# Kernel optimization log

Hardware: AMD Instinct MI355X
Metric: run time of the kernel (lower is better)

Reference implementation:

```python
import jax, jax.numpy as jnp
import numpy as np

B, L, T = 128, 400, 30
E, He, Hd, A, V = 300, 512, 512, 512, 20000
PAD_ID, UNK_ID, SOS_ID = 0, 1, 2


def setup_inputs() -> dict:
    key = jax.random.key(0)
    ks = jax.random.split(key, 20)
    f = lambda k, shape, s=0.05: jax.random.normal(k, shape, jnp.float32) * s
    return {
        "enc_outputs": jax.random.normal(ks[0], (B, L, He), jnp.float32),
        "s": jax.random.normal(ks[1], (B, Hd), jnp.float32),
        "source_WORD_encoding": jax.random.randint(ks[2], (B, L), 0, V),
        "target_WORD_encoding": jax.random.randint(ks[3], (B, T), 0, V),
        "embed": f(ks[4], (V, E)),
        "W_ih": f(ks[5], (3 * Hd, E + He)),
        "b_ih": jnp.zeros((3 * Hd,), jnp.float32),
        "W_hh": f(ks[6], (3 * Hd, Hd)),
        "b_hh": jnp.zeros((3 * Hd,), jnp.float32),
        "att_Wh": f(ks[7], (A, He)),
        "att_Ws": f(ks[8], (A, Hd)),
        "att_b": jnp.zeros((A,), jnp.float32),
        "att_v": f(ks[9], (A,)),
        "copy_W": f(ks[10], (1, He + Hd)),
        "copy_b": jnp.zeros((1,), jnp.float32),
        "read_W": f(ks[11], (Hd, E + He + Hd)),
        "read_b": jnp.zeros((Hd,), jnp.float32),
        "read_Wo": f(ks[12], (V, Hd // 2)),
    }


def reference(enc_outputs, s, source_WORD_encoding, target_WORD_encoding,
              embed, W_ih, b_ih, W_hh, b_hh, att_Wh, att_Ws, att_b, att_v,
              copy_W, copy_b, read_W, read_b, read_Wo):
    pad_mask = source_WORD_encoding == PAD_ID          # [B, L]
    # Precompute encoder projection for Bahdanau attention (same math each step)
    enc_proj = jnp.einsum('ble,ae->bla', enc_outputs, att_Wh)  # [B, L, A]
    word0 = jnp.full((enc_outputs.shape[0],), SOS_ID, jnp.int32)
    ctx0 = jnp.zeros((enc_outputs.shape[0], He), enc_outputs.dtype)

    def step(carry, tgt_t):
        s, ctx, word = carry
        emb = embed[word]                               # [B, E]
        x = jnp.concatenate([emb, ctx], axis=1)         # [B, E+He]
        gi = x @ W_ih.T + b_ih
        gh = s @ W_hh.T + b_hh
        ir, iz, in_ = jnp.split(gi, 3, axis=1)
        hr, hz, hn = jnp.split(gh, 3, axis=1)
        r = jax.nn.sigmoid(ir + hr)
        z = jax.nn.sigmoid(iz + hz)
        n = jnp.tanh(in_ + r * hn)
        s_new = (1.0 - z) * n + z * s                   # GRUCell
        # Bahdanau attention
        q = s_new @ att_Ws.T + att_b                    # [B, A]
        e = jnp.einsum('bla,a->bl', jnp.tanh(enc_proj + q[:, None, :]), att_v)
        e = jnp.where(pad_mask, -jnp.inf, e)
        attn = jax.nn.softmax(e, axis=1)                # [B, L]
        ctx_new = jnp.einsum('bl,ble->be', attn, enc_outputs)
        # Copy switch
        p_copy = jax.nn.sigmoid(jnp.concatenate([s_new, ctx_new], 1) @ copy_W.T + copy_b)
        # Readout (tie=False): Linear -> Maxout(2) -> Wo
        rvec = jnp.concatenate([emb, ctx_new, s_new], 1) @ read_W.T + read_b
        m = rvec.reshape(rvec.shape[0], Hd // 2, 2).max(-1)
        energy = m @ read_Wo.T                          # [B, V]
        p_vocab = jax.nn.softmax(energy, axis=1)
        p_out = jnp.concatenate([(1.0 - p_copy) * p_vocab, p_copy * attn], 1) + 1e-12
        log_p = jnp.log(p_out)                          # [B, V+L]
        next_word = jnp.where(tgt_t >= V, UNK_ID, tgt_t).astype(jnp.int32)
        return (s_new, ctx_new, next_word), log_p

    _, log_ps = jax.lax.scan(step, (s, ctx0, word0), target_WORD_encoding.T.astype(jnp.int32))
    return jnp.transpose(log_ps, (1, 0, 2))             # [B, T, V+L]
```

## Files before the change

kernel.cpp:

```cpp
#include <hip/hip_runtime.h>

typedef unsigned short u16;
typedef unsigned int u32;
typedef short bf16x8 __attribute__((ext_vector_type(8)));
typedef float f32x4 __attribute__((ext_vector_type(4)));

#define NB 128
#define NL 400
#define NT 30
#define NE 300
#define KE 320
#define NHE 512
#define NHD 512
#define NA 512
#define NV 20000
#define NVP 20096
#define K1 1024
#define N1 2048
#define NW 2048
#define OUTW (NV+NL)
#define NBLK 512

static __device__ __forceinline__ u16 f2b(float x){ u32 u=__float_as_uint(x); u += 0x7FFFu + ((u>>16)&1u); return (u16)(u>>16); }
static __device__ __forceinline__ float b2f(u16 h){ return __uint_as_float(((u32)h)<<16); }
static __device__ __forceinline__ float fsig(float x){ return 1.f/(1.f+__expf(-x)); }
static __device__ __forceinline__ float ftanh(float x){ return 1.f - 2.f/(__expf(2.f*x)+1.f); }

static __device__ __forceinline__ float atL(const float* p){ return __hip_atomic_load(p, __ATOMIC_RELAXED, __HIP_MEMORY_SCOPE_AGENT); }
static __device__ __forceinline__ u32   atLu(const u32* p){ return __hip_atomic_load(p, __ATOMIC_RELAXED, __HIP_MEMORY_SCOPE_AGENT); }
static __device__ __forceinline__ void  atS(float* p, float v){ __hip_atomic_store(p, v, __ATOMIC_RELAXED, __HIP_MEMORY_SCOPE_AGENT); }
static __device__ __forceinline__ void  atSu(u32* p, u32 v){ __hip_atomic_store(p, v, __ATOMIC_RELAXED, __HIP_MEMORY_SCOPE_AGENT); }

static __device__ __forceinline__ void gll16(const u16* g, u16* l){
  __builtin_amdgcn_global_load_lds((const __attribute__((address_space(1))) void*)g,
                                   (__attribute__((address_space(3))) void*)l, 16, 0, 0);
}

static __device__ __forceinline__ void gemm_pipe(const u16* A, int lda, const u16* Bm, int ldb,
                                                 int K, u16* ls, f32x4 (&acc)[4][4]){
  const int tid = threadIdx.x;
  const int wave = tid>>6, lane = tid&63;
  const int srow = lane>>2;
  const int sko = (((lane&3) ^ ((lane>>3)&3)))*8;
  const int wm = wave>>1, wn = wave&1;
#pragma unroll
  for (int i=0;i<4;i++)
#pragma unroll
    for (int j=0;j<4;j++)
#pragma unroll
      for (int q=0;q<4;q++) acc[i][j][q] = 0.f;
  const int nk = K>>5;
  auto issue = [&](int kt, int bsel){
    u16* dA = ls + bsel*8192;
    u16* dB = dA + 4096;
#pragma unroll
    for (int i=0;i<2;i++){
      const int c = wave*2+i;
      const int row = c*16 + srow;
      gll16(A + (size_t)row*lda + kt + sko, dA + c*512);
      gll16(Bm + (size_t)row*ldb + kt + sko, dB + c*512);
    }
  };
  issue(0, 0);
  issue(nk>1 ? 32 : 0, 1);
  for (int it=0; it<nk; ++it){
    asm volatile("s_waitcnt vmcnt(4)" ::: "memory");
    __builtin_amdgcn_s_barrier();
    const u16* lsA = ls + (it&1)*8192;
    const u16* lsB = lsA + 4096;
    const int rsel = (lane&15)*32 + (((lane>>4) ^ ((lane>>1)&3))*8);
    bf16x8 aF[4], bF[4];
#pragma unroll
    for (int mi=0;mi<4;mi++) aF[mi] = *(const bf16x8*)(lsA + (wm*64+mi*16)*32 + rsel);
#pragma unroll
    for (int nj=0;nj<4;nj++) bF[nj] = *(const bf16x8*)(lsB + (wn*64+nj*16)*32 + rsel);
#pragma unroll
    for (int mi=0;mi<4;mi++)
#pragma unroll
      for (int nj=0;nj<4;nj++)
        acc[mi][nj] = __builtin_amdgcn_mfma_f32_16x16x32_bf16(aF[mi], bF[nj], acc[mi][nj], 0,0,0);
    __builtin_amdgcn_s_barrier();
    issue(it+2 < nk ? (it+2)*32 : 0, it&1);
  }
  asm volatile("s_waitcnt vmcnt(0)" ::: "memory");
  __builtin_amdgcn_s_barrier();
}


__global__ __launch_bounds__(256) void k_conv_flat(const float* __restrict__ s, u16* __restrict__ d, long n){
  long i = (long)blockIdx.x*256 + threadIdx.x;
  const long st = (long)gridDim.x*256;
  for (; i<n; i+=st) d[i] = f2b(s[i]);
}

__global__ __launch_bounds__(256) void k_convpad(const float* __restrict__ s, u16* __restrict__ d,
                                                 int srows, int sk, int dk, long total){
  long i = (long)blockIdx.x*256 + threadIdx.x;
  const long st = (long)gridDim.x*256;
  for (; i<total; i+=st){
    int r = (int)(i / dk), k = (int)(i - (long)r*dk);
    d[i] = (r < srows && k < sk) ? f2b(s[(size_t)r*sk + k]) : (u16)0;
  }
}

__global__ __launch_bounds__(512) void k_transpose(const float* __restrict__ enc, u16* __restrict__ encT){
  const int b = blockIdx.y, jt = blockIdx.x;
  __shared__ float tile[16][33];
  const int tid = threadIdx.x;
  for (int lt=0; lt<25; lt++){
    {
      int l = lt*16 + (tid>>5), j = jt*32 + (tid&31);
      tile[tid>>5][tid&31] = enc[((size_t)b*NL + l)*512 + j];
    }
    __syncthreads();
    {
      int jw = tid>>4, lw = tid&15;
      encT[((size_t)b*512 + jt*32 + jw)*NL + lt*16 + lw] = f2b(tile[lw][jw]);
    }
    __syncthreads();
  }
}

__global__ __launch_bounds__(256) void k_build_w1(const float* __restrict__ Whh, const float* __restrict__ Wih, u16* __restrict__ d){
  int idx = blockIdx.x*256 + threadIdx.x;
  if (idx >= N1*K1) return;
  int n = idx >> 10, k = idx & 1023;
  float v = 0.f;
  if (n < 1024)       v = (k<512) ? Whh[(size_t)n*512 + k] : Wih[(size_t)n*812 + 300 + (k-512)];
  else if (n < 1536)  v = (k<512) ? Whh[(size_t)n*512 + k] : 0.f;
  else                v = (k<512) ? 0.f : Wih[(size_t)(n-512)*812 + 300 + (k-512)];
  d[idx] = f2b(v);
}

__global__ __launch_bounds__(256) void k_build_w2(const float* __restrict__ Wr, u16* __restrict__ d){
  int idx = blockIdx.x*256 + threadIdx.x;
  if (idx >= 512*K1) return;
  int r = idx >> 10, k = idx & 1023;
  float v = (k<512) ? Wr[(size_t)r*1324 + 812 + k] : Wr[(size_t)r*1324 + 300 + (k-512)];
  d[idx] = f2b(v);
}

__global__ __launch_bounds__(256) void k_build_wemb(const float* __restrict__ Wih, const float* __restrict__ Wr, u16* __restrict__ d){
  int idx = blockIdx.x*256 + threadIdx.x;
  if (idx >= NW*KE) return;
  int n = idx / KE, k = idx - n*KE;
  float v = 0.f;
  if (k < NE) v = (n < 1536) ? Wih[(size_t)n*812 + k] : Wr[(size_t)(n-1536)*1324 + k];
  d[idx] = f2b(v);
}

__global__ __launch_bounds__(256) void k_build_xemb(const int* __restrict__ tgt, const float* __restrict__ embed, u16* __restrict__ d){
  int idx = blockIdx.x*256 + threadIdx.x;
  if (idx >= NT*NB*KE) return;
  int row = idx / KE, k = idx - row*KE;
  int t = row >> 7, b = row & 127;
  u16 hv = 0;
  if (k < NE){
    int w = 2;
    if (t > 0){ w = tgt[b*NT + t-1]; if ((u32)w >= (u32)NV) w = 1; }
    hv = f2b(embed[(size_t)w*NE + k]);
  }
  d[idx] = hv;
}

__global__ __launch_bounds__(256) void k_init(const float* __restrict__ s_in, float* __restrict__ sbuf0, u16* __restrict__ x1A){
  int idx = blockIdx.x*256 + threadIdx.x;
  if (idx < 65536){
    int b = idx>>9, j = idx&511;
    float v = s_in[idx];
    sbuf0[idx] = v;
    x1A[(size_t)b*K1 + j] = f2b(v);
  } else if (idx < 131072){
    int k = idx - 65536;
    int b = k>>9, j = k&511;
    x1A[(size_t)b*K1 + 512 + j] = 0;
  }
}

__global__ __launch_bounds__(256) void k_encproj(const u16* __restrict__ A, const u16* __restrict__ Bw, u16* __restrict__ C){
  __shared__ __align__(16) u16 ls[16384];
  const int n0 = blockIdx.x*128, m0 = blockIdx.y*128;
  f32x4 acc[4][4];
  gemm_pipe(A + (size_t)m0*512, 512, Bw + (size_t)n0*512, 512, 512, ls, acc);
  const int tid=threadIdx.x, wave=tid>>6, lane=tid&63, wm=wave>>1, wn=wave&1;
#pragma unroll
  for (int mi=0;mi<4;mi++)
#pragma unroll
    for (int nj=0;nj<4;nj++)
#pragma unroll
      for (int q=0;q<4;q++){
        int r = m0 + wm*64 + mi*16 + (lane>>4)*4 + q;
        int c = n0 + wn*64 + nj*16 + (lane&15);
        C[(size_t)r*512 + c] = f2b(acc[mi][nj][q]);
      }
}

__global__ __launch_bounds__(256) void k_gemm_emb(const u16* __restrict__ Xe, const u16* __restrict__ We, float* __restrict__ gre){
  __shared__ __align__(16) u16 ls[16384];
  const int n0 = blockIdx.x*128, m0 = blockIdx.y*128;
  f32x4 acc[4][4];
  gemm_pipe(Xe + (size_t)m0*KE, KE, We + (size_t)n0*KE, KE, KE, ls, acc);
  const int tid=threadIdx.x, wave=tid>>6, lane=tid&63, wm=wave>>1, wn=wave&1;
#pragma unroll
  for (int mi=0;mi<4;mi++)
#pragma unroll
    for (int nj=0;nj<4;nj++)
#pragma unroll
      for (int q=0;q<4;q++){
        int r = m0 + wm*64 + mi*16 + (lane>>4)*4 + q;
        int c = n0 + wn*64 + nj*16 + (lane&15);
        gre[(size_t)r*NW + c] = acc[mi][nj][q];
      }
}


struct KP {
  const float *bih, *bhh, *attb, *attv, *copyW, *copyb;
  const int   *src;
  const u16   *Wsb, *eproj, *encT, *W1;
  const float *gre;
  float *gA, *gB, *sbufA, *sbufB, *e, *ctx_ws, *attn_all, *pcb_all;
  u16   *x1A;
  u32   *slots, *gen;
};

static __device__ __forceinline__ void gbar(const KP& p, u32& ep){
  ++ep;
  asm volatile("s_waitcnt vmcnt(0)" ::: "memory");
  __syncthreads();
  if (threadIdx.x==0)
    atSu(p.slots + blockIdx.x, ep);
  if (blockIdx.x==0){
    if (threadIdx.x < 64){
      const u32* sl = p.slots + threadIdx.x*8;
      for (;;){
        u32 mn = 0xFFFFFFFFu;
#pragma unroll
        for (int j=0;j<8;j++){
          u32 v = atLu(sl+j);
          mn = v<mn ? v : mn;
        }
        if (__all(mn >= ep)) break;
        __builtin_amdgcn_s_sleep(4);
      }
      atSu(p.gen + threadIdx.x*16, ep);
    }
  } else if (threadIdx.x==0){
    const u32* gp = p.gen + (blockIdx.x>>3)*16;
    while (atLu(gp) < ep) __builtin_amdgcn_s_sleep(4);
  }
  asm volatile("" ::: "memory");
  __syncthreads();
}

static __device__ void ph_g1(const KP& p, char* sm, int u, int t){
  u16* ls = (u16*)sm;
  const int ks = u&1, n0 = (u>>1)*128;
  const u16* A  = p.x1A + (size_t)t*NB*K1 + ks*512;
  const u16* Bm = p.W1 + (size_t)n0*K1 + ks*512;
  f32x4 acc[4][4];
  gemm_pipe(A, K1, Bm, K1, 512, ls, acc);
  float* gd = ks ? p.gB : p.gA;
  const int tid=threadIdx.x, wave=tid>>6, lane=tid&63, wm=wave>>1, wn=wave&1;
#pragma unroll
  for (int mi=0;mi<4;mi++)
#pragma unroll
    for (int nj=0;nj<4;nj++)
#pragma unroll
      for (int q=0;q<4;q++){
        int r = wm*64 + mi*16 + (lane>>4)*4 + q;
        int c = n0 + wn*64 + nj*16 + (lane&15);
        atS(gd + (size_t)r*N1 + c, acc[mi][nj][q]);
      }
}

static __device__ void ph_gqe(const KP& p, char* sm, int blk, int t){
  const int tid = threadIdx.x;
  const int b = blk>>2, yq = blk&3;
  float* s_lds = (float*)sm;
  float* q_lds = s_lds + 512;
  const float* gAb = p.gA + (size_t)b*N1;
  const float* gBb = p.gB + (size_t)b*N1;
  const float* ge = p.gre + (size_t)(t*NB + b)*NW;
  const float* s_old = (t&1) ? p.sbufB : p.sbufA;
  float* s_new       = (t&1) ? p.sbufA : p.sbufB;
  u16* x1n = p.x1A + (size_t)(t+1)*NB*K1 + (size_t)b*K1;
#pragma unroll
  for (int h=0; h<2; h++){
    const int j = tid + h*256;
    float g0 = atL(gAb + j)      + atL(gBb + j);
    float g1 = atL(gAb + 512+j)  + atL(gBb + 512+j);
    float g2 = atL(gAb + 1024+j) + atL(gBb + 1024+j);
    float g3 = atL(gAb + 1536+j) + atL(gBb + 1536+j);
    float r = fsig(g0 + ge[j] + p.bih[j] + p.bhh[j]);
    float z = fsig(g1 + ge[512+j] + p.bih[512+j] + p.bhh[512+j]);
    float n = ftanh(ge[1024+j] + g3 + p.bih[1024+j] + r*(g2 + p.bhh[1024+j]));
    float sn = (1.f-z)*n + z*atL(s_old + (size_t)b*512 + j);
    s_lds[j] = sn;
    if (yq==0){
      atS(s_new + (size_t)b*512 + j, sn);
      u32 me = f2b(sn);
      u32 oth = (u32)__shfl_xor((int)me, 1);
      if (!(tid&1)) atSu((u32*)(x1n + j), me | (oth<<16));
    }
  }
  __syncthreads();
  {
    const int al = tid>>1, kh = tid&1;
    const int a = yq*128 + al;
    const u16* wr = p.Wsb + (size_t)a*512 + kh*256;
    const float* sp = s_lds + kh*256;
    float acc = 0.f;
#pragma unroll 8
    for (int k=0;k<256;k+=8){
      bf16x8 w = *(const bf16x8*)(wr + k);
#pragma unroll
      for (int j=0;j<8;j++) acc += sp[k+j]*b2f((u16)w[j]);
    }
    acc += __shfl_xor(acc, 1);
    if (kh==0) q_lds[al] = acc + p.attb[a];
  }
  __syncthreads();
  const int lane = tid&63, wv = tid>>6;
  const int g16 = lane>>4, sub = lane&15;
  const int gid = wv*4 + g16;
  float v8[8], q8[8];
#pragma unroll
  for (int j=0;j<8;j++){
    v8[j] = p.attv[yq*128 + sub*8 + j];
    q8[j] = q_lds[sub*8 + j];
  }
  float* epo = p.e + ((size_t)yq*NB + b)*NL;
#pragma unroll 5
  for (int i=0;i<25;i++){
    const int l = i*16 + gid;
    const u16* ep = p.eproj + ((size_t)b*NL + l)*512 + yq*128 + sub*8;
    bf16x8 w8 = *(const bf16x8*)ep;
    float acc = 0.f;
#pragma unroll
    for (int j8=0;j8<8;j8++) acc += v8[j8]*ftanh(b2f((u16)w8[j8]) + q8[j8]);
    acc += __shfl_xor(acc,1); acc += __shfl_xor(acc,2);
    acc += __shfl_xor(acc,4); acc += __shfl_xor(acc,8);
    if (sub==0) atS(epo + l, acc);
  }
}

static __device__ void ph_smctx(const KP& p, char* sm, int blk, int t){
  const int tid = threadIdx.x;
  const int b = blk>>2, jq = blk&3;
  const int lane = tid&63, wv = tid>>6;
  float* a_lds = (float*)sm;
  float* red   = (float*)(sm+1600);
  float* bc    = (float*)(sm+1664);
  float s0 = atL(p.e + (size_t)b*NL + tid)
           + atL(p.e + ((size_t)NB + b)*NL + tid)
           + atL(p.e + ((size_t)2*NB + b)*NL + tid)
           + atL(p.e + ((size_t)3*NB + b)*NL + tid);
  float ev0 = (p.src[b*NL + tid]!=0) ? s0 : -INFINITY;
  float ev1 = -INFINITY;
  if (tid < NL-256){
    float s1 = atL(p.e + (size_t)b*NL + tid+256)
             + atL(p.e + ((size_t)NB + b)*NL + tid+256)
             + atL(p.e + ((size_t)2*NB + b)*NL + tid+256)
             + atL(p.e + ((size_t)3*NB + b)*NL + tid+256);
    ev1 = (p.src[b*NL + tid+256]!=0) ? s1 : -INFINITY;
  }
  float mx = fmaxf(ev0, ev1);
  for (int off=32; off; off>>=1) mx = fmaxf(mx, __shfl_xor(mx, off));
  if (lane==0) red[wv]=mx;
  __syncthreads();
  if (tid==0) bc[0] = fmaxf(fmaxf(red[0],red[1]), fmaxf(red[2],red[3]));
  __syncthreads();
  const float M = bc[0];
  float p0 = (ev0==-INFINITY)? 0.f : __expf(ev0 - M);
  float p1 = (ev1==-INFINITY)? 0.f : __expf(ev1 - M);
  float sm2 = p0 + p1;
  for (int off=32; off; off>>=1) sm2 += __shfl_xor(sm2, off);
  if (lane==0) red[wv]=sm2;
  __syncthreads();
  if (tid==0) bc[1] = red[0]+red[1]+red[2]+red[3];
  __syncthreads();
  const float inv = 1.f / bc[1];
  a_lds[tid] = p0*inv;
  if (tid < NL-256) a_lds[tid+256] = p1*inv;
  __syncthreads();
  if (jq==0){
    float* ab = p.attn_all + ((size_t)t*NB + b)*NL;
    ab[tid] = a_lds[tid];
    if (tid < NL-256) ab[tid+256] = a_lds[tid+256];
  }
  const int j = jq*128 + (tid>>1), lh = tid&1;
  const u16* er = p.encT + ((size_t)b*512 + j)*NL + lh*200;
  const float* ap = a_lds + lh*200;
  float acc = 0.f;
#pragma unroll 5
  for (int m=0;m<200;m+=8){
    bf16x8 e8 = *(const bf16x8*)(er + m);
#pragma unroll
    for (int jj=0;jj<8;jj++) acc += ap[m+jj]*b2f((u16)e8[jj]);
  }
  acc += __shfl_xor(acc, 1);
  u32 me = f2b(acc);
  u32 oth = (u32)__shfl_xor((int)me, 2);
  if ((tid&3)==0)
    atSu((u32*)(p.x1A + (size_t)(t+1)*NB*K1 + (size_t)b*K1 + 512 + j), me | (oth<<16));
  if (!(tid&1)) atS(p.ctx_ws + (size_t)b*512 + j, acc);
}

static __device__ void ph_pcopy(const KP& p, int u, int t){
  const int tid = threadIdx.x;
  const float* sN = (t&1) ? p.sbufA : p.sbufB;
  const int b = u*32 + (tid>>3), kq = tid&7;
  const float* v = (kq<4) ? (sN + (size_t)b*512 + kq*128) : (p.ctx_ws + (size_t)b*512 + (kq-4)*128);
  const float* w = p.copyW + kq*128;
  float acc = 0.f;
#pragma unroll 8
  for (int k=0;k<128;k++) acc += atL(v+k)*w[k];
  acc += __shfl_xor(acc,1); acc += __shfl_xor(acc,2); acc += __shfl_xor(acc,4);
  if (kq==0) p.pcb_all[(size_t)t*NB + b] = fsig(acc + p.copyb[0]);
}

__global__ __launch_bounds__(256,2) void k_persist(KP p){
  __shared__ __align__(16) char sm[33024];
  const int blk = blockIdx.x;
  u32 ep = 0;
  for (int t=0; t<NT; ++t){
    if (blk < 32) ph_g1(p, sm, blk, t);
    else if (blk < 36){ if (t > 0) ph_pcopy(p, blk-32, t-1); }
    gbar(p, ep);
    ph_gqe(p, sm, blk, t);
    gbar(p, ep);
    ph_smctx(p, sm, blk, t);
    gbar(p, ep);
  }
  if (blk < 4) ph_pcopy(p, blk, NT-1);
}


__global__ __launch_bounds__(256) void kB_read(const u16* __restrict__ x1A, const u16* __restrict__ W2,
    const float* __restrict__ gre, const float* __restrict__ readb, u16* __restrict__ mbf_all){
  __shared__ __align__(16) u16 ls[16384];
  const int t = blockIdx.y, n0 = blockIdx.x*128;
  const u16* A = x1A + (size_t)(t+1)*NB*K1;
  f32x4 acc[4][4];
  gemm_pipe(A, K1, W2 + (size_t)n0*K1, K1, K1, ls, acc);
  const int tid=threadIdx.x, wave=tid>>6, lane=tid&63, wm=wave>>1, wn=wave&1;
#pragma unroll
  for (int mi=0;mi<4;mi++)
#pragma unroll
    for (int nj=0;nj<4;nj++)
#pragma unroll
      for (int q=0;q<4;q++){
        int r = wm*64 + mi*16 + (lane>>4)*4 + q;
        int c = n0 + wn*64 + nj*16 + (lane&15);
        float v = acc[mi][nj][q] + readb[c] + gre[((size_t)(t*NB + r))*NW + 1536 + c];
        float o = __shfl_xor(v, 1);
        float mx2 = fmaxf(v, o);
        if (!(lane&1)) mbf_all[(size_t)(t*NB + r)*256 + (c>>1)] = f2b(mx2);
      }
}

__global__ __launch_bounds__(256) void kB_lse(const u16* __restrict__ mbf_all, const u16* __restrict__ WoP,
    float* __restrict__ parts){
  __shared__ __align__(16) u16 ls[16384];
  __shared__ float psum[128][2];
  const int t = blockIdx.y, n0 = blockIdx.x*128;
  f32x4 acc[4][4];
  gemm_pipe(mbf_all + (size_t)t*NB*256, 256, WoP + (size_t)n0*256, 256, 256, ls, acc);
  const int tid=threadIdx.x, wave=tid>>6, lane=tid&63, wm=wave>>1, wn=wave&1;
  float rs[4][4];
#pragma unroll
  for (int mi=0;mi<4;mi++)
#pragma unroll
    for (int q=0;q<4;q++) rs[mi][q]=0.f;
#pragma unroll
  for (int mi=0;mi<4;mi++)
#pragma unroll
    for (int nj=0;nj<4;nj++){
      const int c = n0 + wn*64 + nj*16 + (lane&15);
#pragma unroll
      for (int q=0;q<4;q++)
        if (c < NV) rs[mi][q] += __expf(acc[mi][nj][q]);
    }
#pragma unroll
  for (int mi=0;mi<4;mi++)
#pragma unroll
    for (int q=0;q<4;q++){
      float v = rs[mi][q];
      v += __shfl_xor(v,1); v += __shfl_xor(v,2); v += __shfl_xor(v,4); v += __shfl_xor(v,8);
      if ((lane&15)==0) psum[wm*64 + mi*16 + (lane>>4)*4 + q][wn] = v;
    }
  __syncthreads();
  if (tid < 128) parts[(size_t)(t*NB + tid)*160 + blockIdx.x] = psum[tid][0] + psum[tid][1];
}

__global__ __launch_bounds__(256) void kB_lsered(const float* __restrict__ parts, float* __restrict__ LSE_all){
  const int row = blockIdx.x, tid = threadIdx.x;
  const int lane = tid&63, wv = tid>>6;
  __shared__ float red[4];
  float v = (tid<157)? parts[(size_t)row*160 + tid] : 0.f;
  for (int off=32; off; off>>=1) v += __shfl_xor(v, off);
  if (lane==0) red[wv]=v;
  __syncthreads();
  if (tid==0) LSE_all[row] = __logf(red[0]+red[1]+red[2]+red[3]);
}

__global__ __launch_bounds__(256) void kB_out2(const u16* __restrict__ mbf_all, const u16* __restrict__ WoP,
    const float* __restrict__ LSE_all, const float* __restrict__ pcb_all, float* __restrict__ out){
  __shared__ __align__(16) u16 ls[16384];
  const int t = blockIdx.y, n0 = blockIdx.x*128;
  f32x4 acc[4][4];
  gemm_pipe(mbf_all + (size_t)t*NB*256, 256, WoP + (size_t)n0*256, 256, 256, ls, acc);
  const int tid=threadIdx.x, wave=tid>>6, lane=tid&63, wm=wave>>1, wn=wave&1;
  float lse_r[4][4], lo_r[4][4];
#pragma unroll
  for (int mi=0;mi<4;mi++)
#pragma unroll
    for (int q=0;q<4;q++){
      const int r = wm*64 + mi*16 + (lane>>4)*4 + q;
      lse_r[mi][q] = LSE_all[(size_t)t*NB + r];
      lo_r[mi][q]  = 1.f - pcb_all[(size_t)t*NB + r];
    }
#pragma unroll
  for (int mi=0;mi<4;mi++)
#pragma unroll
    for (int nj=0;nj<4;nj++){
      const int c = n0 + wn*64 + nj*16 + (lane&15);
      if (c >= NV) continue;
#pragma unroll
      for (int q=0;q<4;q++){
        const int r = wm*64 + mi*16 + (lane>>4)*4 + q;
        out[((size_t)r*NT + t)*OUTW + c] = __logf(lo_r[mi][q]*__expf(acc[mi][nj][q]-lse_r[mi][q]) + 1e-12f);
      }
    }
}

__global__ __launch_bounds__(256) void kB_copy(const float* __restrict__ pcb_all, const float* __restrict__ attn_all,
    float* __restrict__ out){
  const int total = NT*NB*NL;
  for (int idx = blockIdx.x*256 + threadIdx.x; idx < total; idx += gridDim.x*256){
    int t = idx / (NB*NL);
    int rem = idx - t*(NB*NL);
    int b = rem / NL, l = rem - b*NL;
    float pc = pcb_all[(size_t)t*NB + b];
    float av = attn_all[((size_t)t*NB + b)*NL + l];
    out[((size_t)b*NT + t)*OUTW + NV + l] = __logf(pc*av + 1e-12f);
  }
}


extern "C" void kernel_launch(void* const* d_in, const int* in_sizes, int n_in,
                              void* d_out, int out_size, void* d_ws, size_t ws_size,
                              hipStream_t stream){
  const float* enc   = (const float*)d_in[0];
  const float* s_in  = (const float*)d_in[1];
  const int*   src   = (const int*)d_in[2];
  const int*   tgt   = (const int*)d_in[3];
  const float* embed = (const float*)d_in[4];
  const float* W_ih  = (const float*)d_in[5];
  const float* b_ih  = (const float*)d_in[6];
  const float* W_hh  = (const float*)d_in[7];
  const float* b_hh  = (const float*)d_in[8];
  const float* attWh = (const float*)d_in[9];
  const float* attWs = (const float*)d_in[10];
  const float* attb  = (const float*)d_in[11];
  const float* attv  = (const float*)d_in[12];
  const float* copyW = (const float*)d_in[13];
  const float* copyb = (const float*)d_in[14];
  const float* readW = (const float*)d_in[15];
  const float* readb = (const float*)d_in[16];
  const float* readWo= (const float*)d_in[17];
  float* out = (float*)d_out;
  (void)in_sizes; (void)n_in; (void)out_size; (void)ws_size;

  char* wsp = (char*)d_ws;
  size_t off = 0;
  auto alloc = [&](size_t bytes)->char*{ char* p = wsp + off; off = (off + bytes + 255) & ~(size_t)255; return p; };
  u16* enc_bf    = (u16*)alloc((size_t)NB*NL*NHE*2);
  u16* encT      = (u16*)alloc((size_t)NB*NHE*NL*2);
  u16* eproj     = (u16*)alloc((size_t)NB*NL*NA*2);
  u16* attWh_bf  = (u16*)alloc((size_t)NA*NHE*2);
  u16* Wsb       = (u16*)alloc((size_t)NA*NHD*2);
  u16* W1        = (u16*)alloc((size_t)N1*K1*2);
  u16* W2        = (u16*)alloc((size_t)512*K1*2);
  u16* Wemb      = (u16*)alloc((size_t)NW*KE*2);
  u16* Xemb      = (u16*)alloc((size_t)NT*NB*KE*2);
  u16* WoP       = (u16*)alloc((size_t)NVP*256*2);
  float* gre     = (float*)alloc((size_t)NT*NB*NW*4);
  float* gA      = (float*)alloc((size_t)NB*N1*4);
  float* gB      = (float*)alloc((size_t)NB*N1*4);
  u16* x1A       = (u16*)alloc((size_t)(NT+1)*NB*K1*2);
  float* sbufA   = (float*)alloc((size_t)NB*NHD*4);
  float* sbufB   = (float*)alloc((size_t)NB*NHD*4);
  float* e_buf   = (float*)alloc((size_t)4*NB*NL*4);
  float* attn_all= (float*)alloc((size_t)NT*NB*NL*4);
  float* ctx_ws  = (float*)alloc((size_t)NB*NHE*4);
  u16* mbf_all   = (u16*)alloc((size_t)NT*NB*256*2);
  float* parts   = (float*)alloc((size_t)NT*NB*160*4);
  float* LSE_all = (float*)alloc((size_t)NT*NB*4);
  float* pcb_all = (float*)alloc((size_t)NT*NB*4);
  u32* slots     = (u32*)alloc((size_t)NBLK*4);
  u32* gen       = (u32*)alloc((size_t)64*64);

  hipMemsetAsync(slots, 0, (size_t)NBLK*4, stream);
  hipMemsetAsync(gen,   0, (size_t)64*64, stream);

  k_conv_flat<<<4096,256,0,stream>>>(enc, enc_bf, (long)NB*NL*NHE);
  k_transpose<<<dim3(16,128),512,0,stream>>>(enc, encT);
  k_conv_flat<<<1024,256,0,stream>>>(attWh, attWh_bf, (long)NA*NHE);
  k_conv_flat<<<1024,256,0,stream>>>(attWs, Wsb, (long)NA*NHD);
  k_build_w1<<<8192,256,0,stream>>>(W_hh, W_ih, W1);
  k_build_w2<<<2048,256,0,stream>>>(readW, W2);
  k_build_wemb<<<2560,256,0,stream>>>(W_ih, readW, Wemb);
  k_build_xemb<<<4800,256,0,stream>>>(tgt, embed, Xemb);
  k_convpad<<<2048,256,0,stream>>>(readWo, WoP, NV, 256, 256, (long)NVP*256);
  k_init<<<512,256,0,stream>>>(s_in, sbufA, x1A);
  k_encproj<<<dim3(4,400),256,0,stream>>>(enc_bf, attWh_bf, eproj);
  k_gemm_emb<<<dim3(16,30),256,0,stream>>>(Xemb, Wemb, gre);

  KP kp;
  kp.bih = b_ih; kp.bhh = b_hh; kp.attb = attb; kp.attv = attv;
  kp.copyW = copyW; kp.copyb = copyb;
  kp.src = src;
  kp.Wsb = Wsb; kp.eproj = eproj; kp.encT = encT; kp.W1 = W1;
  kp.gre = gre;
  kp.gA = gA; kp.gB = gB; kp.sbufA = sbufA; kp.sbufB = sbufB;
  kp.e = e_buf; kp.ctx_ws = ctx_ws; kp.attn_all = attn_all; kp.pcb_all = pcb_all;
  kp.x1A = x1A;
  kp.slots = slots; kp.gen = gen;

  k_persist<<<NBLK,256,0,stream>>>(kp);

  kB_read<<<dim3(4,NT),256,0,stream>>>(x1A, W2, gre, readb, mbf_all);
  kB_lse<<<dim3(157,NT),256,0,stream>>>(mbf_all, WoP, parts);
  kB_lsered<<<NT*NB,256,0,stream>>>(parts, LSE_all);
  kB_out2<<<dim3(157,NT),256,0,stream>>>(mbf_all, WoP, LSE_all, pcb_all, out);
  kB_copy<<<1024,256,0,stream>>>(pcb_all, attn_all, out);
}
```

Before: 3.139 ms.

## Double persistent grid to 1024 blocks and split attention work finer

Raises the persistent kernel's block count from 512 to 1024 and the occupancy hint to 4 blocks per CU. The attention-score phase now splits the 400 source positions across two blocks, and the context phase has each block cover 64 output features with a 4-way split over positions. The grid barrier is widened to match. The goal is more parallel work per step on the serial decode loop. The cost is a barrier over twice as many blocks, duplicated GRU and query computation per block, and pressure on registers and LDS to fit 4 blocks per CU.

```diff
diff --git a/kernel.cpp b/kernel.cpp
--- a/kernel.cpp
+++ b/kernel.cpp
@@ -19,7 +19,7 @@
 #define N1 2048
 #define NW 2048
 #define OUTW (NV+NL)
-#define NBLK 512
+#define NBLK 1024
 
 static __device__ __forceinline__ u16 f2b(float x){ u32 u=__float_as_uint(x); u += 0x7FFFu + ((u>>16)&1u); return (u16)(u>>16); }
 static __device__ __forceinline__ float b2f(u16 h){ return __uint_as_float(((u32)h)<<16); }
@@ -232,11 +232,11 @@
     atSu(p.slots + blockIdx.x, ep);
   if (blockIdx.x==0){
     if (threadIdx.x < 64){
-      const u32* sl = p.slots + threadIdx.x*8;
+      const u32* sl = p.slots + threadIdx.x*16;
       for (;;){
         u32 mn = 0xFFFFFFFFu;
 #pragma unroll
-        for (int j=0;j<8;j++){
+        for (int j=0;j<16;j++){
           u32 v = atLu(sl+j);
           mn = v<mn ? v : mn;
         }
@@ -246,7 +246,7 @@
       atSu(p.gen + threadIdx.x*16, ep);
     }
   } else if (threadIdx.x==0){
-    const u32* gp = p.gen + (blockIdx.x>>3)*16;
+    const u32* gp = p.gen + (blockIdx.x>>4)*16;
     while (atLu(gp) < ep) __builtin_amdgcn_s_sleep(4);
   }
   asm volatile("" ::: "memory");
@@ -276,7 +276,7 @@
 
 static __device__ void ph_gqe(const KP& p, char* sm, int blk, int t){
   const int tid = threadIdx.x;
-  const int b = blk>>2, yq = blk&3;
+  const int b = blk>>3, yq = (blk>>1)&3, lh = blk&1;
   float* s_lds = (float*)sm;
   float* q_lds = s_lds + 512;
   const float* gAb = p.gA + (size_t)b*N1;
@@ -297,7 +297,7 @@
     float n = ftanh(ge[1024+j] + g3 + p.bih[1024+j] + r*(g2 + p.bhh[1024+j]));
     float sn = (1.f-z)*n + z*atL(s_old + (size_t)b*512 + j);
     s_lds[j] = sn;
-    if (yq==0){
+    if ((blk&7)==0){
       atS(s_new + (size_t)b*512 + j, sn);
       u32 me = f2b(sn);
       u32 oth = (u32)__shfl_xor((int)me, 1);
@@ -331,8 +331,8 @@
     q8[j] = q_lds[sub*8 + j];
   }
   float* epo = p.e + ((size_t)yq*NB + b)*NL;
-#pragma unroll 5
-  for (int i=0;i<25;i++){
+  const int i0 = lh ? 13 : 0, i1 = lh ? 25 : 13;
+  for (int i=i0;i<i1;i++){
     const int l = i*16 + gid;
     const u16* ep = p.eproj + ((size_t)b*NL + l)*512 + yq*128 + sub*8;
     bf16x8 w8 = *(const bf16x8*)ep;
@@ -347,7 +347,7 @@
 
 static __device__ void ph_smctx(const KP& p, char* sm, int blk, int t){
   const int tid = threadIdx.x;
-  const int b = blk>>2, jq = blk&3;
+  const int b = blk>>3, yo = blk&7;
   const int lane = tid&63, wv = tid>>6;
   float* a_lds = (float*)sm;
   float* red   = (float*)(sm+1600);
@@ -384,27 +384,28 @@
   a_lds[tid] = p0*inv;
   if (tid < NL-256) a_lds[tid+256] = p1*inv;
   __syncthreads();
-  if (jq==0){
+  if (yo==0){
     float* ab = p.attn_all + ((size_t)t*NB + b)*NL;
     ab[tid] = a_lds[tid];
     if (tid < NL-256) ab[tid+256] = a_lds[tid+256];
   }
-  const int j = jq*128 + (tid>>1), lh = tid&1;
-  const u16* er = p.encT + ((size_t)b*512 + j)*NL + lh*200;
-  const float* ap = a_lds + lh*200;
+  const int j = yo*64 + (tid>>2), lq = tid&3;
+  const int l0 = lq*104;
+  const int nm = (lq<3) ? 13 : 11;
+  const u16* er = p.encT + ((size_t)b*512 + j)*NL + l0;
+  const float* ap = a_lds + l0;
   float acc = 0.f;
-#pragma unroll 5
-  for (int m=0;m<200;m+=8){
-    bf16x8 e8 = *(const bf16x8*)(er + m);
-#pragma unroll
-    for (int jj=0;jj<8;jj++) acc += ap[m+jj]*b2f((u16)e8[jj]);
-  }
-  acc += __shfl_xor(acc, 1);
+  for (int m=0;m<nm;m++){
+    bf16x8 e8 = *(const bf16x8*)(er + m*8);
+#pragma unroll
+    for (int jj=0;jj<8;jj++) acc += ap[m*8+jj]*b2f((u16)e8[jj]);
+  }
+  acc += __shfl_xor(acc,1); acc += __shfl_xor(acc,2);
   u32 me = f2b(acc);
-  u32 oth = (u32)__shfl_xor((int)me, 2);
-  if ((tid&3)==0)
+  u32 oth = (u32)__shfl_xor((int)me, 4);
+  if ((tid&7)==0)
     atSu((u32*)(p.x1A + (size_t)(t+1)*NB*K1 + (size_t)b*K1 + 512 + j), me | (oth<<16));
-  if (!(tid&1)) atS(p.ctx_ws + (size_t)b*512 + j, acc);
+  if ((tid&3)==0) atS(p.ctx_ws + (size_t)b*512 + j, acc);
 }
 
 static __device__ void ph_pcopy(const KP& p, int u, int t){
@@ -420,7 +421,7 @@
   if (kq==0) p.pcb_all[(size_t)t*NB + b] = fsig(acc + p.copyb[0]);
 }
 
-__global__ __launch_bounds__(256,2) void k_persist(KP p){
+__global__ __launch_bounds__(256,4) void k_persist(KP p){
   __shared__ __align__(16) char sm[33024];
   const int blk = blockIdx.x;
   u32 ep = 0;
```

Result: slower. 4.278 ms (+36.3%).
